# Optimization experiments

Measured on AMD Instinct MI355X. Metric: run time of the kernel, lower is better.

## Reference

```python
import jax, jax.numpy as jnp
import numpy as np

B, N, M = 8, 4096, 4096


def setup_inputs() -> dict:
    key = jax.random.key(0)
    ks = jax.random.split(key, 8)
    return {
        "x_aligned": jax.random.normal(ks[0], (B, N, 3), dtype=jnp.float32),
        "y": jax.random.normal(ks[1], (B, M, 3), dtype=jnp.float32),
        "R": jax.random.normal(ks[2], (B, 3, 3), dtype=jnp.float32),
        "S": jax.random.normal(ks[3], (B, 3), dtype=jnp.float32),
        "t": jax.random.normal(ks[4], (B, 3, 1), dtype=jnp.float32),
        "R_gt": jax.random.normal(ks[5], (B, 3, 3), dtype=jnp.float32),
        "S_gt": jax.random.normal(ks[6], (B, 3), dtype=jnp.float32),
        "t_gt": jax.random.normal(ks[7], (B, 3), dtype=jnp.float32),
    }


def chamfer_distance(x, y):
    # x: [B,N,3], y: [B,M,3]; bidirectional mean squared NN distance
    xn = jnp.sum(x * x, axis=-1)                      # [B,N]
    yn = jnp.sum(y * y, axis=-1)                      # [B,M]
    xy = jnp.einsum('bnd,bmd->bnm', x, y)             # [B,N,M]
    d2 = xn[:, :, None] + yn[:, None, :] - 2.0 * xy   # [B,N,M] squared dists
    cham_x = jnp.mean(jnp.min(d2, axis=2), axis=1)    # [B] x -> y
    cham_y = jnp.mean(jnp.min(d2, axis=1), axis=1)    # [B] y -> x
    return jnp.mean(cham_x) + jnp.mean(cham_y)        # batch mean, summed dirs


def reference(x_aligned, y, R, S, t, R_gt, S_gt, t_gt):
    t = jnp.squeeze(t)                                # [B,3]
    eye = jnp.eye(3, dtype=R.dtype)
    R_loss = jnp.einsum('bij,bkj->bik', R, R_gt) - eye  # R @ R_gt^T - I
    L_reg = (jnp.sum(R_loss * R_loss)
             + jnp.sum((S - S_gt) ** 2)
             + jnp.sum((t - t_gt) ** 2))
    L_chamfer = chamfer_distance(x_aligned, y)
    return L_reg + L_chamfer
```

## Files before the change

### kernel.cpp

```cpp
#include <hip/hip_runtime.h>

#define BB 8
#define NN 4096
#define MC 256
#define NCHUNK (NN / MC)
#define KPT 8
#define TPB 256
#define PTS_PER_BLOCK (TPB * KPT)
#define NPTS (2 * BB * NN)


__global__ __launch_bounds__(TPB) void chamfer_partial(
    const float* __restrict__ X, const float* __restrict__ Y,
    float* __restrict__ partial) {
  __shared__ float4 ly[MC];
  const int tid = threadIdx.x;
  const int zb  = blockIdx.z;
  const int b   = zb & (BB - 1);
  const int dir = zb >> 3;
  const float* pts  = dir ? (Y + b * NN * 3) : (X + b * NN * 3);
  const float* refs = dir ? (X + b * NN * 3) : (Y + b * NN * 3);
  const int c = blockIdx.y;

  {
    const int j = c * MC + tid;
    const float a0 = refs[j * 3 + 0];
    const float a1 = refs[j * 3 + 1];
    const float a2 = refs[j * 3 + 2];
    ly[tid] = make_float4(-2.0f * a0, -2.0f * a1, -2.0f * a2,
                          a0 * a0 + a1 * a1 + a2 * a2);
  }
  __syncthreads();

  float px[KPT], py[KPT], pz[KPT], m[KPT];
  const int p0 = blockIdx.x * PTS_PER_BLOCK + tid;
#pragma unroll
  for (int k = 0; k < KPT; k++) {
    const int p = p0 + k * TPB;
    px[k] = pts[p * 3 + 0];
    py[k] = pts[p * 3 + 1];
    pz[k] = pts[p * 3 + 2];
    m[k] = 1e30f;
  }

#pragma unroll 2
  for (int j = 0; j < MC; j += 2) {
    const float4 w0 = ly[j];
    const float4 w1 = ly[j + 1];
#pragma unroll
    for (int k = 0; k < KPT; k++) {
      const float s0 = fmaf(px[k], w0.x, fmaf(py[k], w0.y, fmaf(pz[k], w0.z, w0.w)));
      const float s1 = fmaf(px[k], w1.x, fmaf(py[k], w1.y, fmaf(pz[k], w1.z, w1.w)));
      m[k] = fminf(m[k], fminf(s0, s1));
    }
  }

#pragma unroll
  for (int k = 0; k < KPT; k++) {
    const int p = p0 + k * TPB;
    const float pn = px[k] * px[k] + py[k] * py[k] + pz[k] * pz[k];
    partial[(c * (2 * BB) + zb) * NN + p] = m[k] + pn;
  }
}

__global__ __launch_bounds__(256) void chamfer_reduce(
    const float* __restrict__ partial,
    const float* __restrict__ R, const float* __restrict__ S,
    const float* __restrict__ t, const float* __restrict__ Rgt,
    const float* __restrict__ Sgt, const float* __restrict__ tgt,
    float* __restrict__ out) {
  const int tid = threadIdx.x;
  const int q0 = blockIdx.x * 1024 + tid;
  float s = 0.0f;
#pragma unroll
  for (int kk = 0; kk < 4; kk++) {
    const int q = q0 + kk * 256;
    float m = 1e30f;
#pragma unroll
    for (int c = 0; c < NCHUNK; c++)
      m = fminf(m, partial[c * NPTS + q]);
    s += m;
  }
  for (int o = 32; o > 0; o >>= 1) s += __shfl_down(s, o);
  __shared__ float wsum[4];
  if ((tid & 63) == 0) wsum[tid >> 6] = s;
  __syncthreads();
  if (tid == 0) {
    const float bs = wsum[0] + wsum[1] + wsum[2] + wsum[3];
    atomicAdd(out, bs * (1.0f / (float)(BB * NN)));
  }

  if (blockIdx.x == 0) {
    float v = 0.0f;
    if (tid < 72) {
      const int b = tid / 9, ik = tid % 9, i = ik / 3, k = ik % 3;
      const float* Rb = R + b * 9;
      const float* Gb = Rgt + b * 9;
      float d = Rb[i * 3 + 0] * Gb[k * 3 + 0] +
                Rb[i * 3 + 1] * Gb[k * 3 + 1] +
                Rb[i * 3 + 2] * Gb[k * 3 + 2];
      d -= (i == k) ? 1.0f : 0.0f;
      v = d * d;
    } else if (tid < 96) {
      const int i = tid - 72;
      const float d = S[i] - Sgt[i];
      v = d * d;
    } else if (tid < 120) {
      const int i = tid - 96;
      const float d = t[i] - tgt[i];
      v = d * d;
    }
    for (int o = 32; o > 0; o >>= 1) v += __shfl_down(v, o);
    __shared__ float rsum[4];
    if ((tid & 63) == 0) rsum[tid >> 6] = v;
    __syncthreads();
    if (tid == 0) atomicAdd(out, rsum[0] + rsum[1] + rsum[2] + rsum[3]);
  }
}

extern "C" void kernel_launch(void* const* d_in, const int* in_sizes, int n_in,
                              void* d_out, int out_size, void* d_ws, size_t ws_size,
                              hipStream_t stream) {
  const float* X   = (const float*)d_in[0];
  const float* Y   = (const float*)d_in[1];
  const float* R   = (const float*)d_in[2];
  const float* S   = (const float*)d_in[3];
  const float* t   = (const float*)d_in[4];
  const float* Rgt = (const float*)d_in[5];
  const float* Sgt = (const float*)d_in[6];
  const float* tgt = (const float*)d_in[7];

  float* partial = (float*)d_ws;
  float* out     = (float*)d_out;

  hipMemsetAsync(out, 0, sizeof(float), stream);

  dim3 gA(NN / PTS_PER_BLOCK, NCHUNK, 2 * BB);
  chamfer_partial<<<gA, TPB, 0, stream>>>(X, Y, partial);

  chamfer_reduce<<<NPTS / 1024, 256, 0, stream>>>(partial, R, S, t, Rgt, Sgt, tgt, out);
}
```

Baseline: 97.62 us.

## Use packed FP32 FMA over paired reference points and double points per thread

Evaluates two reference points per instruction with v_pk_fma_f32, storing the references in shared memory as a pair-interleaved SoA layout. Points per thread go from 8 to 16, so each block covers the whole point set and the grid shrinks from 2 to 1 block in x. The point loads are also moved ahead of the barrier. The aim is to cut VALU instruction count and LDS traffic per pair evaluated. In exchange, register pressure roughly doubles, and with only 256 blocks in total occupancy and parallelism may drop.

Measured after the change: 104.6 us. 1.07x slower.

```diff
diff --git a/kernel.cpp b/kernel.cpp
--- a/kernel.cpp
+++ b/kernel.cpp
@@ -4,16 +4,25 @@
 #define NN 4096
 #define MC 256
 #define NCHUNK (NN / MC)
-#define KPT 8
+#define KPT 16
 #define TPB 256
 #define PTS_PER_BLOCK (TPB * KPT)
 #define NPTS (2 * BB * NN)
 
 
+typedef __attribute__((ext_vector_type(2))) float f2;
+
+__device__ __forceinline__ f2 pk_fma(f2 a, f2 b, f2 c) {
+  f2 d;
+  asm("v_pk_fma_f32 %0, %1, %2, %3" : "=v"(d) : "v"(a), "v"(b), "v"(c));
+  return d;
+}
+
 __global__ __launch_bounds__(TPB) void chamfer_partial(
     const float* __restrict__ X, const float* __restrict__ Y,
     float* __restrict__ partial) {
-  __shared__ float4 ly[MC];
+  __shared__ float4 lxy[MC / 2];
+  __shared__ float4 lzw[MC / 2];
   const int tid = threadIdx.x;
   const int zb  = blockIdx.z;
   const int b   = zb & (BB - 1);
@@ -22,43 +31,53 @@
   const float* refs = dir ? (X + b * NN * 3) : (Y + b * NN * 3);
   const int c = blockIdx.y;
 
-  {
-    const int j = c * MC + tid;
-    const float a0 = refs[j * 3 + 0];
-    const float a1 = refs[j * 3 + 1];
-    const float a2 = refs[j * 3 + 2];
-    ly[tid] = make_float4(-2.0f * a0, -2.0f * a1, -2.0f * a2,
-                          a0 * a0 + a1 * a1 + a2 * a2);
+  if (tid < MC / 2) {
+    const int j = c * MC + 2 * tid;
+    const float a0 = refs[j * 3 + 0], a1 = refs[j * 3 + 1], a2 = refs[j * 3 + 2];
+    const float b0 = refs[j * 3 + 3], b1 = refs[j * 3 + 4], b2 = refs[j * 3 + 5];
+    lxy[tid] = make_float4(-2.0f * a0, -2.0f * b0, -2.0f * a1, -2.0f * b1);
+    lzw[tid] = make_float4(-2.0f * a2, -2.0f * b2,
+                           a0 * a0 + a1 * a1 + a2 * a2,
+                           b0 * b0 + b1 * b1 + b2 * b2);
+  }
+
+  f2 px2[KPT], py2[KPT], pz2[KPT];
+  float m[KPT];
+#pragma unroll
+  for (int k = 0; k < KPT; k++) {
+    const int p = tid + k * TPB;
+    const float qx = pts[p * 3 + 0];
+    const float qy = pts[p * 3 + 1];
+    const float qz = pts[p * 3 + 2];
+    px2[k] = (f2){qx, qx};
+    py2[k] = (f2){qy, qy};
+    pz2[k] = (f2){qz, qz};
+    m[k] = 1e30f;
   }
   __syncthreads();
 
-  float px[KPT], py[KPT], pz[KPT], m[KPT];
-  const int p0 = blockIdx.x * PTS_PER_BLOCK + tid;
-#pragma unroll
-  for (int k = 0; k < KPT; k++) {
-    const int p = p0 + k * TPB;
-    px[k] = pts[p * 3 + 0];
-    py[k] = pts[p * 3 + 1];
-    pz[k] = pts[p * 3 + 2];
-    m[k] = 1e30f;
-  }
-
 #pragma unroll 2
-  for (int j = 0; j < MC; j += 2) {
-    const float4 w0 = ly[j];
-    const float4 w1 = ly[j + 1];
+  for (int jp = 0; jp < MC / 2; jp++) {
+    const float4 wxy = lxy[jp];
+    const float4 wzw = lzw[jp];
+    const f2 xp = (f2){wxy.x, wxy.y};
+    const f2 yp = (f2){wxy.z, wxy.w};
+    const f2 zp = (f2){wzw.x, wzw.y};
+    const f2 wp = (f2){wzw.z, wzw.w};
 #pragma unroll
     for (int k = 0; k < KPT; k++) {
-      const float s0 = fmaf(px[k], w0.x, fmaf(py[k], w0.y, fmaf(pz[k], w0.z, w0.w)));
-      const float s1 = fmaf(px[k], w1.x, fmaf(py[k], w1.y, fmaf(pz[k], w1.z, w1.w)));
-      m[k] = fminf(m[k], fminf(s0, s1));
+      f2 s = pk_fma(pz2[k], zp, wp);
+      s = pk_fma(py2[k], yp, s);
+      s = pk_fma(px2[k], xp, s);
+      m[k] = fminf(m[k], fminf(s.x, s.y));
     }
   }
 
 #pragma unroll
   for (int k = 0; k < KPT; k++) {
-    const int p = p0 + k * TPB;
-    const float pn = px[k] * px[k] + py[k] * py[k] + pz[k] * pz[k];
+    const int p = tid + k * TPB;
+    const float qx = px2[k].x, qy = py2[k].x, qz = pz2[k].x;
+    const float pn = qx * qx + qy * qy + qz * qz;
     partial[(c * (2 * BB) + zb) * NN + p] = m[k] + pn;
   }
 }
@@ -135,7 +154,7 @@
 
   hipMemsetAsync(out, 0, sizeof(float), stream);
 
-  dim3 gA(NN / PTS_PER_BLOCK, NCHUNK, 2 * BB);
+  dim3 gA(1, NCHUNK, 2 * BB);
   chamfer_partial<<<gA, TPB, 0, stream>>>(X, Y, partial);
 
   chamfer_reduce<<<NPTS / 1024, 256, 0, stream>>>(partial, R, S, t, Rgt, Sgt, tgt, out);
```
